# Kernel optimization log

Measured on AMD Instinct MI355X. Metric: run time of the kernel, lower is better.

Reference implementation:

```python
import jax, jax.numpy as jnp
import numpy as np

B, LQ, LT, D = 16, 576, 512, 768
H, DH = 12, 64
TOPK = 64
GATE_INIT = -4.0
EPS = 1e-5


def _layernorm(x, g, b):
    m = jnp.mean(x, axis=-1, keepdims=True)
    v = jnp.mean(jnp.square(x - m), axis=-1, keepdims=True)
    return (x - m) * jax.lax.rsqrt(v + EPS) * g + b


def setup_inputs() -> dict:
    key = jax.random.key(0)
    ks = jax.random.split(key, 8)
    s = D ** -0.5
    return {
        "x_q": jax.random.normal(ks[0], (B, LQ, D), jnp.float32),
        "x_kv": jax.random.normal(ks[1], (B, LT, D), jnp.float32),
        "kv_attn_mask": jnp.ones((B, LT), jnp.int32),
        "wq": jax.random.normal(ks[2], (D, D), jnp.float32) * s,
        "wk": jax.random.normal(ks[3], (D, D), jnp.float32) * s,
        "wv": jax.random.normal(ks[4], (D, D), jnp.float32) * s,
        "wo": jax.random.normal(ks[5], (D, D), jnp.float32) * s,
        "ln_q_g": jnp.ones((D,), jnp.float32),
        "ln_q_b": jnp.zeros((D,), jnp.float32),
        "ln_kv_g": jnp.ones((D,), jnp.float32),
        "ln_kv_b": jnp.zeros((D,), jnp.float32),
        "head_queries": jax.random.normal(ks[6], (H, DH), jnp.float32) * DH ** -0.5,
        "resid_logit": jnp.asarray(GATE_INIT, jnp.float32),
    }


def reference(x_q, x_kv, kv_attn_mask, wq, wk, wv, wo,
              ln_q_g, ln_q_b, ln_kv_g, ln_kv_b, head_queries, resid_logit):
    scale = DH ** -0.5
    Bc, Lq, _ = x_q.shape
    Lt = x_kv.shape[1]
    xq_n = _layernorm(x_q, ln_q_g, ln_q_b)
    xkv_n = _layernorm(x_kv, ln_kv_g, ln_kv_b)
    # torch Linear: y = x @ W.T
    q = (xq_n @ wq.T).reshape(Bc, Lq, H, DH).transpose(0, 2, 1, 3)   # [B,H,Lq,DH]
    k = (xkv_n @ wk.T).reshape(Bc, Lt, H, DH).transpose(0, 2, 1, 3)  # [B,H,Lt,DH]
    v = (xkv_n @ wv.T).reshape(Bc, Lt, H, DH).transpose(0, 2, 1, 3)

    valid = (kv_attn_mask != 0)  # [B,Lt]
    neg = jnp.asarray(-jnp.inf, q.dtype)

    # head-wise gate from learned head queries attending over keys
    gate_scores = jnp.einsum('hd,bhld->bhl', head_queries, k) * scale  # [B,H,Lt]
    gate_scores = jnp.where(valid[:, None, :], gate_scores, neg)
    gate_attn = jax.nn.softmax(gate_scores, axis=-1)
    c_h = jnp.einsum('bhl,bhld->bhd', gate_attn, k)
    g_logits = jnp.einsum('bhd,hd->bh', c_h, head_queries) * scale
    g_h = jax.nn.sigmoid(g_logits)[:, :, None, None]  # [B,H,1,1]

    # top-k token routing: zero out non-selected K/V (matches torch.where -> zeros)
    if TOPK and TOPK < Lt:
        _, topk_idx = jax.lax.top_k(gate_scores, TOPK)  # [B,H,K]
        keep = jax.nn.one_hot(topk_idx, Lt, dtype=q.dtype).sum(axis=-2) > 0  # [B,H,Lt]
        k = jnp.where(keep[..., None], k, 0.0)
        v = jnp.where(keep[..., None], v, 0.0)

    attn_logits = jnp.einsum('bhqd,bhkd->bhqk', q, k) * scale  # [B,H,Lq,Lt]
    attn_logits = jnp.where(valid[:, None, None, :], attn_logits, neg)
    attn = jax.nn.softmax(attn_logits, axis=-1)
    out = jnp.einsum('bhqk,bhkd->bhqd', attn, v) * g_h
    out = out.transpose(0, 2, 1, 3).reshape(Bc, Lq, H * DH)
    out = out @ wo.T
    alpha = jax.nn.sigmoid(resid_logit)
    return x_q + alpha * out
```

## Files before the change

kernel.cpp:

```cpp
#include <hip/hip_runtime.h>
#include <math.h>

#define BB 16
#define LQ 576
#define LT 512
#define DD 768
#define HH 12
#define DH 64
#define TOPK 64

typedef __attribute__((ext_vector_type(8))) short bf16x8;
typedef __attribute__((ext_vector_type(4))) float f32x4;
typedef __attribute__((ext_vector_type(4))) unsigned short u16x4;

static constexpr size_t XQBF  = 0;
static constexpr size_t XKVBF = 3538944;
static constexpr size_t WQB   = 6684672;
static constexpr size_t WKB   = 6979584;
static constexpr size_t WVB   = 7274496;
static constexpr size_t WOB   = 7569408;
static constexpr size_t QBFo  = 7864320;
static constexpr size_t UBo   = 11403264;
static constexpr size_t GSo   = 11409408;
static constexpr size_t IDXo  = 17694720;
static constexpr size_t VBIA  = 17707008;
static constexpr size_t NDVo  = 17719296;
static constexpr size_t GHo   = 17719488;
static constexpr size_t KCo   = 17719680;
static constexpr size_t VCTo  = 18112896;

__device__ inline unsigned short f2bf(float f) {
  union { float f; unsigned u; } v; v.f = f;
  unsigned r = v.u + 0x7FFFu + ((v.u >> 16) & 1u);
  return (unsigned short)(r >> 16);
}
__device__ inline float bf2f(unsigned short u) {
  union { unsigned u; float f; } v; v.u = ((unsigned)u) << 16;
  return v.f;
}
__device__ inline void gload_lds16(const void* src, void* dst) {
  __builtin_amdgcn_global_load_lds((const __attribute__((address_space(1))) void*)src,
                                   (__attribute__((address_space(3))) void*)dst, 16, 0, 0);
}

__global__ __launch_bounds__(256) void ln_all(const float* __restrict__ xq,
                                              const float* __restrict__ xkv,
                                              const float* __restrict__ gq,
                                              const float* __restrict__ bq,
                                              const float* __restrict__ gkv,
                                              const float* __restrict__ bkv,
                                              unsigned short* __restrict__ yq,
                                              unsigned short* __restrict__ ykv) {
  int row = blockIdx.x;
  const float *xr, *gg, *bb;
  unsigned short* yr;
  if (row < BB * LQ) {
    xr = xq + (size_t)row * DD; gg = gq; bb = bq; yr = yq + (size_t)row * DD;
  } else {
    int r = row - BB * LQ;
    xr = xkv + (size_t)r * DD; gg = gkv; bb = bkv; yr = ykv + (size_t)r * DD;
  }
  int t = threadIdx.x;
  float v0 = xr[t], v1 = xr[t + 256], v2 = xr[t + 512];
  __shared__ float red[4];
  float s = v0 + v1 + v2;
  #pragma unroll
  for (int o = 32; o > 0; o >>= 1) s += __shfl_xor(s, o);
  if ((t & 63) == 0) red[t >> 6] = s;
  __syncthreads();
  float m = (red[0] + red[1] + red[2] + red[3]) * (1.0f / 768.0f);
  float d0 = v0 - m, d1 = v1 - m, d2 = v2 - m;
  float s2 = d0 * d0 + d1 * d1 + d2 * d2;
  #pragma unroll
  for (int o = 32; o > 0; o >>= 1) s2 += __shfl_xor(s2, o);
  __syncthreads();
  if ((t & 63) == 0) red[t >> 6] = s2;
  __syncthreads();
  float var = (red[0] + red[1] + red[2] + red[3]) * (1.0f / 768.0f);
  float rs = rsqrtf(var + 1e-5f);
  yr[t]       = f2bf(d0 * rs * gg[t]       + bb[t]);
  yr[t + 256] = f2bf(d1 * rs * gg[t + 256] + bb[t + 256]);
  yr[t + 512] = f2bf(d2 * rs * gg[t + 512] + bb[t + 512]);
}

__global__ __launch_bounds__(256) void conv4u(const float* __restrict__ s0, const float* __restrict__ s1,
                                              const float* __restrict__ s2, const float* __restrict__ s3,
                                              unsigned short* d0, unsigned short* d1,
                                              unsigned short* d2, unsigned short* d3,
                                              const float* __restrict__ hq,
                                              unsigned short* __restrict__ UB) {
  int t = threadIdx.x;
  if (blockIdx.y == 4) {
    int h = blockIdx.x;
    if (h >= 16) return;
    if (h < HH) {
      float a0 = 0.0f, a1 = 0.0f, a2 = 0.0f;
      for (int d = 0; d < DH; ++d) {
        float sc = hq[h * DH + d];
        const float* wr = s1 + (size_t)(h * DH + d) * DD;
        a0 += sc * wr[t]; a1 += sc * wr[t + 256]; a2 += sc * wr[t + 512];
      }
      UB[h * DD + t]       = f2bf(a0 * 0.125f);
      UB[h * DD + t + 256] = f2bf(a1 * 0.125f);
      UB[h * DD + t + 512] = f2bf(a2 * 0.125f);
    } else {
      UB[h * DD + t] = 0; UB[h * DD + t + 256] = 0; UB[h * DD + t + 512] = 0;
    }
    return;
  }
  const float* s; unsigned short* d;
  switch (blockIdx.y) {
    case 0: s = s0; d = d0; break;
    case 1: s = s1; d = d1; break;
    case 2: s = s2; d = d2; break;
    default: s = s3; d = d3; break;
  }
  int i = (blockIdx.x * 256 + t) * 4;
  float4 v = *reinterpret_cast<const float4*>(&s[i]);
  u16x4 o = { f2bf(v.x), f2bf(v.y), f2bf(v.z), f2bf(v.w) };
  *reinterpret_cast<u16x4*>(&d[i]) = o;
}


#define COMMON_PREAMBLE()                                                      \
  const int tid = threadIdx.x;                                                 \
  const int w = tid >> 6, l = tid & 63;                                        \
  const int lq = l & 15, g = l >> 4;                                           \
  const int srow = l >> 3;                                                     \
  const int scol = ((l & 7) * 16) ^ ((srow & 7) << 4);

#define STAGE2(BUFI, T)                                                        \
  {                                                                            \
    int k0s = (T) * 64;                                                        \
    _Pragma("unroll")                                                          \
    for (int it = 0; it < 4; ++it) {                                           \
      int rbase = it * 32 + w * 8;                                             \
      gload_lds16(Asrc + (size_t)rbase * DD + k0s, &As[BUFI][rbase * 64]);     \
      gload_lds16(Bsrc + (size_t)rbase * DD + k0s, &Bs[BUFI][rbase * 64]);     \
    }                                                                          \
  }

#define COMPUTE2(BUFI)                                                         \
  {                                                                            \
    bf16x8 a[4][2], b[4][2];                                                   \
    _Pragma("unroll")                                                          \
    for (int mi = 0; mi < 4; ++mi)                                             \
      _Pragma("unroll")                                                        \
      for (int ks = 0; ks < 2; ++ks) {                                         \
        a[mi][ks] = *reinterpret_cast<const bf16x8*>(&As[BUFI][aoff[mi][ks]]); \
        b[mi][ks] = *reinterpret_cast<const bf16x8*>(&Bs[BUFI][boff[mi][ks]]); \
      }                                                                        \
    _Pragma("unroll")                                                          \
    for (int ks = 0; ks < 2; ++ks)                                             \
      _Pragma("unroll")                                                        \
      for (int mi = 0; mi < 4; ++mi)                                           \
        _Pragma("unroll")                                                      \
        for (int ni = 0; ni < 4; ++ni)                                         \
          acc[mi][ni] = __builtin_amdgcn_mfma_f32_16x16x32_bf16(               \
              a[mi][ks], b[ni][ks], acc[mi][ni], 0, 0, 0);                     \
  }

#define GEMM_MAIN()                                                            \
  int aoff[4][2], boff[4][2];                                                  \
  _Pragma("unroll")                                                            \
  for (int mi = 0; mi < 4; ++mi) {                                             \
    int rowa = wr * 64 + mi * 16 + lq;                                         \
    int rowb = wc * 64 + mi * 16 + lq;                                         \
    _Pragma("unroll")                                                          \
    for (int ks = 0; ks < 2; ++ks) {                                           \
      aoff[mi][ks] = rowa * 64 + (((ks * 64 + g * 16) ^ ((rowa & 7) << 4)) >> 1); \
      boff[mi][ks] = rowb * 64 + (((ks * 64 + g * 16) ^ ((rowb & 7) << 4)) >> 1); \
    }                                                                          \
  }                                                                            \
  STAGE2(0, 0);                                                                \
  STAGE2(1, 1);                                                                \
  _Pragma("unroll")                                                            \
  for (int t = 0; t < 12; ++t) {                                               \
    if (t < 11) asm volatile("s_waitcnt vmcnt(8)" ::: "memory");               \
    else        asm volatile("s_waitcnt vmcnt(0)" ::: "memory");               \
    __builtin_amdgcn_sched_barrier(0);                                         \
    __builtin_amdgcn_s_barrier();                                              \
    if ((t & 1) == 0) { COMPUTE2(0); } else { COMPUTE2(1); }                   \
    __builtin_amdgcn_s_barrier();                                              \
    __builtin_amdgcn_sched_barrier(0);                                         \
    if (t + 2 < 12) {                                                          \
      if ((t & 1) == 0) { STAGE2(0, t + 2); } else { STAGE2(1, t + 2); }       \
    }                                                                          \
  }

__global__ __launch_bounds__(256) void gs_gemm(const unsigned short* __restrict__ xkvb,
                                               const unsigned short* __restrict__ UB,
                                               float* __restrict__ GS) {
  __shared__ __align__(16) unsigned short Xs[2][64 * 64];
  __shared__ __align__(16) unsigned short Us[2][16 * 64];
  COMMON_PREAMBLE();
  const int bm = blockIdx.x * 64;
  const unsigned short* Asrc = xkvb + (size_t)(bm + srow) * DD + (scol >> 1);
  const unsigned short* Us0 = UB + (size_t)srow * DD + (scol >> 1);
  const unsigned short* Us1 = UB + (size_t)(8 + srow) * DD + (scol >> 1);

#define GS_STAGE(BUFI, T)                                                      \
  {                                                                            \
    int k0s = (T) * 64;                                                        \
    _Pragma("unroll")                                                          \
    for (int it = 0; it < 2; ++it) {                                           \
      int rbase = it * 32 + w * 8;                                             \
      gload_lds16(Asrc + (size_t)rbase * DD + k0s, &Xs[BUFI][rbase * 64]);     \
    }                                                                          \
    gload_lds16(Us0 + k0s, &Us[BUFI][0]);                                      \
    gload_lds16(Us1 + k0s, &Us[BUFI][8 * 64]);                                 \
  }

  f32x4 acc = {};

#define GS_COMPUTE(BUFI)                                                       \
  {                                                                            \
    _Pragma("unroll")                                                          \
    for (int ks = 0; ks < 2; ++ks) {                                           \
      int arow = w * 16 + lq;                                                  \
      int acb = (ks * 64 + g * 16) ^ ((arow & 7) << 4);                        \
      bf16x8 a = *reinterpret_cast<const bf16x8*>(&Xs[BUFI][arow * 64 + (acb >> 1)]); \
      int brow = lq;                                                           \
      int bcb = (ks * 64 + g * 16) ^ ((brow & 7) << 4);                        \
      bf16x8 b = *reinterpret_cast<const bf16x8*>(&Us[BUFI][brow * 64 + (bcb >> 1)]); \
      acc = __builtin_amdgcn_mfma_f32_16x16x32_bf16(a, b, acc, 0, 0, 0);       \
    }                                                                          \
  }

  GS_STAGE(0, 0);
  GS_STAGE(1, 1);
  #pragma unroll
  for (int t = 0; t < 12; ++t) {
    if (t < 11) asm volatile("s_waitcnt vmcnt(4)" ::: "memory");
    else        asm volatile("s_waitcnt vmcnt(0)" ::: "memory");
    __builtin_amdgcn_sched_barrier(0);
    __builtin_amdgcn_s_barrier();
    if ((t & 1) == 0) { GS_COMPUTE(0); } else { GS_COMPUTE(1); }
    __builtin_amdgcn_s_barrier();
    __builtin_amdgcn_sched_barrier(0);
    if (t + 2 < 12) {
      if ((t & 1) == 0) { GS_STAGE(0, t + 2); } else { GS_STAGE(1, t + 2); }
    }
  }
  #pragma unroll
  for (int r = 0; r < 4; ++r)
    GS[(size_t)(bm + w * 16 + g * 4 + r) * 16 + lq] = acc[r];
}

__global__ __launch_bounds__(512) void gate_topk(const float* __restrict__ GS,
                                                 const int* __restrict__ mask,
                                                 int* __restrict__ idxo,
                                                 float* __restrict__ vbias,
                                                 float* __restrict__ ndv,
                                                 float* __restrict__ g_h) {
  int bh = blockIdx.x, b = bh / HH, h = bh % HH;
  int l = threadIdx.x;
  __shared__ float s_sc[512];
  __shared__ float red[8];
  __shared__ int wred[8];
  float sc = GS[(size_t)(b * LT + l) * 16 + h];
  bool maskv = (mask[b * LT + l] != 0);
  if (!maskv) sc = -INFINITY;
  s_sc[l] = sc;
  float m0 = sc;
  #pragma unroll
  for (int o = 32; o > 0; o >>= 1) m0 = fmaxf(m0, __shfl_xor(m0, o));
  if ((l & 63) == 0) red[l >> 6] = m0;
  __syncthreads();
  float m = red[0];
  #pragma unroll
  for (int w = 1; w < 8; w++) m = fmaxf(m, red[w]);
  float p = __expf(sc - m);
  float s1 = p;
  #pragma unroll
  for (int o = 32; o > 0; o >>= 1) s1 += __shfl_xor(s1, o);
  __syncthreads();
  if ((l & 63) == 0) red[l >> 6] = s1;
  __syncthreads();
  float Z = 0.0f;
  #pragma unroll
  for (int w = 0; w < 8; w++) Z += red[w];
  p /= Z;
  float gc = maskv ? p * sc : 0.0f;
  #pragma unroll
  for (int o = 32; o > 0; o >>= 1) gc += __shfl_xor(gc, o);
  __syncthreads();
  if ((l & 63) == 0) red[l >> 6] = gc;
  __syncthreads();
  if (l == 0) {
    float G = 0.0f;
    #pragma unroll
    for (int w = 0; w < 8; w++) G += red[w];
    g_h[bh] = 1.0f / (1.0f + __expf(-G));
  }
  float my = s_sc[l];
  int cnt = 0;
  for (int j = 0; j < LT; j++) {
    float sj = s_sc[j];
    cnt += (sj > my || (sj == my && j < l)) ? 1 : 0;
  }
  if (cnt < TOPK) {
    idxo[bh * TOPK + cnt] = l;
    vbias[bh * TOPK + cnt] = maskv ? 0.0f : -INFINITY;
  }
  int dv = (maskv && cnt >= TOPK) ? 1 : 0;
  unsigned long long bal = __ballot(dv);
  if ((l & 63) == 0) wred[l >> 6] = __popcll(bal);
  __syncthreads();
  if (l == 0) {
    int nd = 0;
    #pragma unroll
    for (int w = 0; w < 8; w++) nd += wred[w];
    ndv[bh] = (float)nd;
  }
}

__global__ __launch_bounds__(256, 2) void proj2(const unsigned short* __restrict__ xqb,
                                                const unsigned short* __restrict__ wqb,
                                                const unsigned short* __restrict__ xkvb,
                                                const unsigned short* __restrict__ wkb,
                                                const unsigned short* __restrict__ wvb,
                                                const int* __restrict__ idxo,
                                                unsigned short* __restrict__ QBF,
                                                unsigned short* __restrict__ KC,
                                                unsigned short* __restrict__ VCT) {
  __shared__ __align__(16) unsigned short As[2][128 * 64];
  __shared__ __align__(16) unsigned short Bs[2][128 * 64];
  __shared__ int sidx[64];
  COMMON_PREAMBLE();
  int p = blockIdx.x;
  int bid = (p & 7) * 78 + (p >> 3);

  if (bid < 432) {
    const int wr = w >> 1, wc = w & 1;
    const int mtile = bid / 6, nt = bid % 6;
    const int bm = mtile * 128, bn = nt * 128;
    const unsigned short* Asrc = xqb + (size_t)(bm + srow) * DD + (scol >> 1);
    const unsigned short* Bsrc = wqb + (size_t)(bn + srow) * DD + (scol >> 1);
    f32x4 acc[4][4] = {};
    GEMM_MAIN();
    const int m_base = bm + wr * 64, n_base = bn + wc * 64;
    #pragma unroll
    for (int mi = 0; mi < 4; ++mi)
      #pragma unroll
      for (int r = 0; r < 4; ++r) {
        int m = m_base + mi * 16 + g * 4 + r;
        #pragma unroll
        for (int ni = 0; ni < 4; ++ni) {
          int n = n_base + ni * 16 + lq;
          QBF[(size_t)m * DD + n] = f2bf(acc[mi][ni][r] * 0.125f);
        }
      }
  } else {
    const int bh = bid - 432, b = bh / HH, h = bh % HH;
    if (tid < 64) sidx[tid] = idxo[bh * TOPK + tid];
    __syncthreads();
    unsigned short* Xs0 = &As[0][0]; unsigned short* Xs1 = &As[0][4096];
    unsigned short* Kp0 = &As[1][0]; unsigned short* Kp1 = &As[1][4096];
    unsigned short* Vp0 = &Bs[0][0]; unsigned short* Vp1 = &Bs[0][4096];
    const int j0 = w * 16 + srow, j1 = w * 16 + 8 + srow;
    const unsigned short* xs0 = xkvb + (size_t)(b * LT + sidx[j0]) * DD + (scol >> 1);
    const unsigned short* xs1 = xkvb + (size_t)(b * LT + sidx[j1]) * DD + (scol >> 1);
    const unsigned short* wk0 = wkb + (size_t)(h * DH + j0) * DD + (scol >> 1);
    const unsigned short* wk1 = wkb + (size_t)(h * DH + j1) * DD + (scol >> 1);
    const unsigned short* wv0 = wvb + (size_t)(h * DH + j0) * DD + (scol >> 1);
    const unsigned short* wv1 = wvb + (size_t)(h * DH + j1) * DD + (scol >> 1);

#define KV_STAGE(Xd, Kd, Vd, T)                                                \
    {                                                                          \
      int k0s = (T) * 64;                                                      \
      gload_lds16(xs0 + k0s, Xd + (w * 16) * 64);                              \
      gload_lds16(xs1 + k0s, Xd + (w * 16 + 8) * 64);                          \
      gload_lds16(wk0 + k0s, Kd + (w * 16) * 64);                              \
      gload_lds16(wk1 + k0s, Kd + (w * 16 + 8) * 64);                          \
      gload_lds16(wv0 + k0s, Vd + (w * 16) * 64);                              \
      gload_lds16(wv1 + k0s, Vd + (w * 16 + 8) * 64);                          \
    }

    f32x4 accK[4] = {}, accV[4] = {};

#define KV_COMPUTE(Xd, Kd, Vd)                                                 \
    {                                                                          \
      _Pragma("unroll")                                                        \
      for (int ks = 0; ks < 2; ++ks) {                                         \
        int arow = w * 16 + lq;                                                \
        int acb = (ks * 64 + g * 16) ^ ((arow & 7) << 4);                      \
        bf16x8 ax = *reinterpret_cast<const bf16x8*>(&Xd[arow * 64 + (acb >> 1)]); \
        bf16x8 av = *reinterpret_cast<const bf16x8*>(&Vd[arow * 64 + (acb >> 1)]); \
        _Pragma("unroll")                                                      \
        for (int ni = 0; ni < 4; ++ni) {                                       \
          int brow = ni * 16 + lq;                                             \
          int bcb = (ks * 64 + g * 16) ^ ((brow & 7) << 4);                    \
          bf16x8 bk = *reinterpret_cast<const bf16x8*>(&Kd[brow * 64 + (bcb >> 1)]); \
          accK[ni] = __builtin_amdgcn_mfma_f32_16x16x32_bf16(ax, bk, accK[ni], 0, 0, 0); \
          bf16x8 bx = *reinterpret_cast<const bf16x8*>(&Xd[brow * 64 + (bcb >> 1)]); \
          accV[ni] = __builtin_amdgcn_mfma_f32_16x16x32_bf16(av, bx, accV[ni], 0, 0, 0); \
        }                                                                      \
      }                                                                        \
    }

    KV_STAGE(Xs0, Kp0, Vp0, 0);
    KV_STAGE(Xs1, Kp1, Vp1, 1);
    #pragma unroll
    for (int t = 0; t < 12; ++t) {
      if (t < 11) asm volatile("s_waitcnt vmcnt(6)" ::: "memory");
      else        asm volatile("s_waitcnt vmcnt(0)" ::: "memory");
      __builtin_amdgcn_sched_barrier(0);
      __builtin_amdgcn_s_barrier();
      if ((t & 1) == 0) { KV_COMPUTE(Xs0, Kp0, Vp0); } else { KV_COMPUTE(Xs1, Kp1, Vp1); }
      __builtin_amdgcn_s_barrier();
      __builtin_amdgcn_sched_barrier(0);
      if (t + 2 < 12) {
        if ((t & 1) == 0) { KV_STAGE(Xs0, Kp0, Vp0, t + 2); } else { KV_STAGE(Xs1, Kp1, Vp1, t + 2); }
      }
    }
    #pragma unroll
    for (int ni = 0; ni < 4; ++ni)
      #pragma unroll
      for (int r = 0; r < 4; ++r) {
        int mrow = w * 16 + g * 4 + r;
        KC [(size_t)bh * 4096 + mrow * 64 + ni * 16 + lq] = f2bf(accK[ni][r]);
        VCT[(size_t)bh * 4096 + mrow * 64 + ni * 16 + lq] = f2bf(accV[ni][r]);
      }
  }
}

__global__ __launch_bounds__(256, 2) void o_gemm(const unsigned short* __restrict__ ABF,
                                                 const unsigned short* __restrict__ wob,
                                                 float* __restrict__ out,
                                                 const float* __restrict__ resid,
                                                 const float* __restrict__ gl) {
  __shared__ __align__(16) unsigned short As[2][128 * 64];
  __shared__ __align__(16) unsigned short Bs[2][128 * 64];
  COMMON_PREAMBLE();
  const int wr = w >> 1, wc = w & 1;
  int p = blockIdx.x;
  int bid = (p & 7) * 54 + (p >> 3);
  const int mtile = bid / 6, nt = bid % 6;
  const int bm = mtile * 128, bn = nt * 128;
  const unsigned short* Asrc = ABF + (size_t)(bm + srow) * DD + (scol >> 1);
  const unsigned short* Bsrc = wob + (size_t)(bn + srow) * DD + (scol >> 1);

  f32x4 acc[4][4] = {};
  GEMM_MAIN();

  float alpha = 1.0f / (1.0f + __expf(-gl[0]));
  const int m_base = bm + wr * 64, n_base = bn + wc * 64;
  #pragma unroll
  for (int mi = 0; mi < 4; ++mi)
    #pragma unroll
    for (int r = 0; r < 4; ++r) {
      int m = m_base + mi * 16 + g * 4 + r;
      #pragma unroll
      for (int ni = 0; ni < 4; ++ni) {
        int n = n_base + ni * 16 + lq;
        out[(size_t)m * DD + n] = resid[(size_t)m * DD + n] + alpha * acc[mi][ni][r];
      }
    }
}

__global__ __launch_bounds__(256) void attn_topk(const unsigned short* __restrict__ Qb,
                                                 const unsigned short* __restrict__ KC,
                                                 const unsigned short* __restrict__ VCT,
                                                 const float* __restrict__ vbias,
                                                 const float* __restrict__ ndv,
                                                 const float* __restrict__ g_h,
                                                 unsigned short* __restrict__ att) {
  const int bh = blockIdx.y, b = bh / HH, h = bh % HH;
  const int q0 = blockIdx.x * 64;
  const int tid = threadIdx.x;
  const int w = tid >> 6, l = tid & 63;
  const int lq = l & 15, g = l >> 4;

  __shared__ __align__(16) unsigned short Klds[64 * 64];
  __shared__ __align__(16) unsigned short Vlds[64 * 64];
  __shared__ float svb[64];

  const int srow = l >> 3;
  const int scol = ((l & 7) * 16) ^ ((srow & 7) << 4);
  #pragma unroll
  for (int it = 0; it < 2; ++it) {
    int rbase = w * 16 + it * 8;
    gload_lds16(KC  + (size_t)bh * 4096 + (rbase + srow) * 64 + (scol >> 1), &Klds[rbase * 64]);
    gload_lds16(VCT + (size_t)bh * 4096 + (rbase + srow) * 64 + (scol >> 1), &Vlds[rbase * 64]);
  }
  if (tid < 64) svb[tid] = vbias[bh * TOPK + tid];

  bf16x8 qf0, qf1;
  {
    const unsigned short* qrow =
        Qb + ((size_t)(b * LQ + q0 + w * 16 + lq)) * DD + h * DH + g * 8;
    qf0 = *reinterpret_cast<const bf16x8*>(qrow);
    qf1 = *reinterpret_cast<const bf16x8*>(qrow + 32);
  }
  __syncthreads();

  f32x4 S[4];
  #pragma unroll
  for (int kt = 0; kt < 4; ++kt) {
    f32x4 acc = {};
    int row = kt * 16 + lq;
    int c0 = (g * 16) ^ ((row & 7) << 4);
    int c1 = (64 + g * 16) ^ ((row & 7) << 4);
    bf16x8 a0 = *reinterpret_cast<const bf16x8*>(&Klds[row * 64 + (c0 >> 1)]);
    bf16x8 a1 = *reinterpret_cast<const bf16x8*>(&Klds[row * 64 + (c1 >> 1)]);
    acc = __builtin_amdgcn_mfma_f32_16x16x32_bf16(a0, qf0, acc, 0, 0, 0);
    acc = __builtin_amdgcn_mfma_f32_16x16x32_bf16(a1, qf1, acc, 0, 0, 0);
    S[kt] = acc;
  }

  float s_v[16];
  float mx = -INFINITY;
  #pragma unroll
  for (int kt = 0; kt < 4; ++kt)
    #pragma unroll
    for (int r = 0; r < 4; ++r) {
      float s = S[kt][r] + svb[kt * 16 + g * 4 + r];
      s_v[kt * 4 + r] = s;
      mx = fmaxf(mx, s);
    }
  mx = fmaxf(mx, __shfl_xor(mx, 16));
  mx = fmaxf(mx, __shfl_xor(mx, 32));
  float nd = ndv[bh];
  float m2 = (nd > 0.0f) ? fmaxf(mx, 0.0f) : mx;

  float psum = 0.0f;
  unsigned short pb[16];
  #pragma unroll
  for (int i = 0; i < 16; ++i) {
    float p = __expf(s_v[i] - m2);
    psum += p;
    pb[i] = f2bf(p);
  }
  psum += __shfl_xor(psum, 16);
  psum += __shfl_xor(psum, 32);
  float Z = psum + nd * __expf(-m2);
  float inv = 1.0f / Z;

  bf16x8 pa0, pa1;
  #pragma unroll
  for (int j = 0; j < 8; ++j) { pa0[j] = (short)pb[j]; pa1[j] = (short)pb[8 + j]; }

  f32x4 O[4] = {};
  #pragma unroll
  for (int dt = 0; dt < 4; ++dt) {
    int r = dt * 16 + lq;
    int swz = (r & 7) << 4;
    #pragma unroll
    for (int ks = 0; ks < 2; ++ks) {
      int cl = (64 * ks + g * 8) ^ swz;
      int ch = (64 * ks + 32 + g * 8) ^ swz;
      u16x4 lo = *reinterpret_cast<const u16x4*>(&Vlds[r * 64 + (cl >> 1)]);
      u16x4 hi = *reinterpret_cast<const u16x4*>(&Vlds[r * 64 + (ch >> 1)]);
      bf16x8 vb = { (short)lo[0], (short)lo[1], (short)lo[2], (short)lo[3],
                    (short)hi[0], (short)hi[1], (short)hi[2], (short)hi[3] };
      O[dt] = __builtin_amdgcn_mfma_f32_16x16x32_bf16(ks == 0 ? pa0 : pa1, vb, O[dt], 0, 0, 0);
    }
  }

  float invl[4];
  #pragma unroll
  for (int r = 0; r < 4; ++r) invl[r] = __shfl(inv, g * 4 + r);
  float gh = g_h[bh];
  #pragma unroll
  for (int dt = 0; dt < 4; ++dt)
    #pragma unroll
    for (int r = 0; r < 4; ++r) {
      int q = q0 + w * 16 + g * 4 + r;
      att[((size_t)(b * LQ + q)) * DD + h * DH + dt * 16 + lq] =
          f2bf(O[dt][r] * invl[r] * gh);
    }
}

extern "C" void kernel_launch(void* const* d_in, const int* in_sizes, int n_in,
                              void* d_out, int out_size, void* d_ws, size_t ws_size,
                              hipStream_t stream) {
  const float* x_q      = (const float*)d_in[0];
  const float* x_kv     = (const float*)d_in[1];
  const int*   mask     = (const int*)d_in[2];
  const float* wq       = (const float*)d_in[3];
  const float* wk       = (const float*)d_in[4];
  const float* wv       = (const float*)d_in[5];
  const float* wo       = (const float*)d_in[6];
  const float* ln_q_g   = (const float*)d_in[7];
  const float* ln_q_b   = (const float*)d_in[8];
  const float* ln_kv_g  = (const float*)d_in[9];
  const float* ln_kv_b  = (const float*)d_in[10];
  const float* hq       = (const float*)d_in[11];
  const float* resid_l  = (const float*)d_in[12];
  float* out = (float*)d_out;
  float* ws  = (float*)d_ws;

  unsigned short* xqb  = (unsigned short*)(ws + XQBF);
  unsigned short* xkvb = (unsigned short*)(ws + XKVBF);
  unsigned short* wqb  = (unsigned short*)(ws + WQB);
  unsigned short* wkb  = (unsigned short*)(ws + WKB);
  unsigned short* wvb  = (unsigned short*)(ws + WVB);
  unsigned short* wob  = (unsigned short*)(ws + WOB);
  unsigned short* QBF  = (unsigned short*)(ws + QBFo);
  unsigned short* UB   = (unsigned short*)(ws + UBo);
  float*          GS   = (float*)(ws + GSo);
  int*            IDX  = (int*)(ws + IDXo);
  unsigned short* KC   = (unsigned short*)(ws + KCo);
  unsigned short* VCT  = (unsigned short*)(ws + VCTo);
  unsigned short* ABF  = xqb;

  conv4u<<<dim3(576, 5), dim3(256), 0, stream>>>(wq, wk, wv, wo, wqb, wkb, wvb, wob, hq, UB);

  ln_all<<<dim3(BB * LQ + BB * LT), dim3(256), 0, stream>>>(x_q, x_kv, ln_q_g, ln_q_b,
                                                            ln_kv_g, ln_kv_b, xqb, xkvb);

  gs_gemm<<<dim3(128), dim3(256), 0, stream>>>(xkvb, UB, GS);

  gate_topk<<<dim3(BB * HH), dim3(512), 0, stream>>>(GS, mask, IDX,
                                                     ws + VBIA, ws + NDVo, ws + GHo);

  proj2<<<dim3(624), dim3(256), 0, stream>>>(xqb, wqb, xkvb, wkb, wvb, IDX, QBF, KC, VCT);

  attn_topk<<<dim3(LQ / 64, BB * HH), dim3(256), 0, stream>>>(QBF, KC, VCT,
                                                              ws + VBIA, ws + NDVo, ws + GHo, ABF);

  o_gemm<<<dim3(432), dim3(256), 0, stream>>>(ABF, wob, out, x_q, resid_l);
}
```

Baseline: 110.5 us.

## Split fused Q/KV projection kernel and shrink Q/O GEMM tiles to 64x128

The fused proj2 kernel, which ran the Q projection and the gathered top-k K/V projection in one launch, is split into a dedicated q_gemm and a separate kvc_gemm. Q and O GEMMs now use 64x128 tiles with each wave computing 32x64, which doubles the block count to 864 and raises the occupancy hint to 3 blocks per CU. The aim is better load balance and more waves in flight on the many-CU device. In exchange it adds an extra kernel launch and lowers per-block data reuse because the tiles are smaller.

```diff
diff --git a/kernel.cpp b/kernel.cpp
--- a/kernel.cpp
+++ b/kernel.cpp
@@ -121,7 +121,6 @@
   *reinterpret_cast<u16x4*>(&d[i]) = o;
 }
 
-
 #define COMMON_PREAMBLE()                                                      \
   const int tid = threadIdx.x;                                                 \
   const int w = tid >> 6, l = tid & 63;                                        \
@@ -129,64 +128,132 @@
   const int srow = l >> 3;                                                     \
   const int scol = ((l & 7) * 16) ^ ((srow & 7) << 4);
 
-#define STAGE2(BUFI, T)                                                        \
+
+#define QO_STAGE(BUFI, T)                                                      \
   {                                                                            \
     int k0s = (T) * 64;                                                        \
     _Pragma("unroll")                                                          \
-    for (int it = 0; it < 4; ++it) {                                           \
-      int rbase = it * 32 + w * 8;                                             \
-      gload_lds16(Asrc + (size_t)rbase * DD + k0s, &As[BUFI][rbase * 64]);     \
-      gload_lds16(Bsrc + (size_t)rbase * DD + k0s, &Bs[BUFI][rbase * 64]);     \
-    }                                                                          \
-  }
-
-#define COMPUTE2(BUFI)                                                         \
+    for (int it = 0; it < 2; ++it)                                             \
+      gload_lds16(Asrc + (size_t)it * 8 * DD + k0s, &As[BUFI][(w * 16 + it * 8) * 64]); \
+    _Pragma("unroll")                                                          \
+    for (int jt = 0; jt < 4; ++jt)                                             \
+      gload_lds16(Bsrc + (size_t)jt * 8 * DD + k0s, &Bs[BUFI][(w * 32 + jt * 8) * 64]); \
+  }
+
+#define QO_COMPUTE(BUFI)                                                       \
   {                                                                            \
-    bf16x8 a[4][2], b[4][2];                                                   \
-    _Pragma("unroll")                                                          \
-    for (int mi = 0; mi < 4; ++mi)                                             \
+    bf16x8 a[2][2], b[4][2];                                                   \
+    _Pragma("unroll")                                                          \
+    for (int mi = 0; mi < 2; ++mi)                                             \
       _Pragma("unroll")                                                        \
-      for (int ks = 0; ks < 2; ++ks) {                                         \
+      for (int ks = 0; ks < 2; ++ks)                                           \
         a[mi][ks] = *reinterpret_cast<const bf16x8*>(&As[BUFI][aoff[mi][ks]]); \
-        b[mi][ks] = *reinterpret_cast<const bf16x8*>(&Bs[BUFI][boff[mi][ks]]); \
-      }                                                                        \
+    _Pragma("unroll")                                                          \
+    for (int ni = 0; ni < 4; ++ni)                                             \
+      _Pragma("unroll")                                                        \
+      for (int ks = 0; ks < 2; ++ks)                                           \
+        b[ni][ks] = *reinterpret_cast<const bf16x8*>(&Bs[BUFI][boff[ni][ks]]); \
     _Pragma("unroll")                                                          \
     for (int ks = 0; ks < 2; ++ks)                                             \
       _Pragma("unroll")                                                        \
-      for (int mi = 0; mi < 4; ++mi)                                           \
+      for (int mi = 0; mi < 2; ++mi)                                           \
         _Pragma("unroll")                                                      \
         for (int ni = 0; ni < 4; ++ni)                                         \
           acc[mi][ni] = __builtin_amdgcn_mfma_f32_16x16x32_bf16(               \
               a[mi][ks], b[ni][ks], acc[mi][ni], 0, 0, 0);                     \
   }
 
-#define GEMM_MAIN()                                                            \
-  int aoff[4][2], boff[4][2];                                                  \
+#define QO_MAIN()                                                              \
+  const int wr = w >> 1, wc = w & 1;                                           \
+  int aoff[2][2], boff[4][2];                                                  \
   _Pragma("unroll")                                                            \
-  for (int mi = 0; mi < 4; ++mi) {                                             \
-    int rowa = wr * 64 + mi * 16 + lq;                                         \
-    int rowb = wc * 64 + mi * 16 + lq;                                         \
-    _Pragma("unroll")                                                          \
-    for (int ks = 0; ks < 2; ++ks) {                                           \
+  for (int mi = 0; mi < 2; ++mi) {                                             \
+    int rowa = wr * 32 + mi * 16 + lq;                                         \
+    _Pragma("unroll")                                                          \
+    for (int ks = 0; ks < 2; ++ks)                                             \
       aoff[mi][ks] = rowa * 64 + (((ks * 64 + g * 16) ^ ((rowa & 7) << 4)) >> 1); \
-      boff[mi][ks] = rowb * 64 + (((ks * 64 + g * 16) ^ ((rowb & 7) << 4)) >> 1); \
-    }                                                                          \
   }                                                                            \
-  STAGE2(0, 0);                                                                \
-  STAGE2(1, 1);                                                                \
+  _Pragma("unroll")                                                            \
+  for (int ni = 0; ni < 4; ++ni) {                                             \
+    int rowb = wc * 64 + ni * 16 + lq;                                         \
+    _Pragma("unroll")                                                          \
+    for (int ks = 0; ks < 2; ++ks)                                             \
+      boff[ni][ks] = rowb * 64 + (((ks * 64 + g * 16) ^ ((rowb & 7) << 4)) >> 1); \
+  }                                                                            \
+  QO_STAGE(0, 0);                                                              \
+  QO_STAGE(1, 1);                                                              \
   _Pragma("unroll")                                                            \
   for (int t = 0; t < 12; ++t) {                                               \
-    if (t < 11) asm volatile("s_waitcnt vmcnt(8)" ::: "memory");               \
+    if (t < 11) asm volatile("s_waitcnt vmcnt(6)" ::: "memory");               \
     else        asm volatile("s_waitcnt vmcnt(0)" ::: "memory");               \
     __builtin_amdgcn_sched_barrier(0);                                         \
     __builtin_amdgcn_s_barrier();                                              \
-    if ((t & 1) == 0) { COMPUTE2(0); } else { COMPUTE2(1); }                   \
+    if ((t & 1) == 0) { QO_COMPUTE(0); } else { QO_COMPUTE(1); }               \
     __builtin_amdgcn_s_barrier();                                              \
     __builtin_amdgcn_sched_barrier(0);                                         \
     if (t + 2 < 12) {                                                          \
-      if ((t & 1) == 0) { STAGE2(0, t + 2); } else { STAGE2(1, t + 2); }       \
+      if ((t & 1) == 0) { QO_STAGE(0, t + 2); } else { QO_STAGE(1, t + 2); }   \
     }                                                                          \
   }
+
+__global__ __launch_bounds__(256, 3) void q_gemm(const unsigned short* __restrict__ xqb,
+                                                 const unsigned short* __restrict__ wqb,
+                                                 unsigned short* __restrict__ QBF) {
+  __shared__ __align__(16) unsigned short As[2][64 * 64];
+  __shared__ __align__(16) unsigned short Bs[2][128 * 64];
+  COMMON_PREAMBLE();
+  int p = blockIdx.x;
+  int bid = (p & 7) * 108 + (p >> 3);
+  const int mtile = bid / 6, nt = bid % 6;
+  const int bm = mtile * 64, bn = nt * 128;
+  const unsigned short* Asrc = xqb + (size_t)(bm + w * 16 + srow) * DD + (scol >> 1);
+  const unsigned short* Bsrc = wqb + (size_t)(bn + w * 32 + srow) * DD + (scol >> 1);
+  f32x4 acc[2][4] = {};
+  QO_MAIN();
+  const int m_base = bm + wr * 32, n_base = bn + wc * 64;
+  #pragma unroll
+  for (int mi = 0; mi < 2; ++mi)
+    #pragma unroll
+    for (int r = 0; r < 4; ++r) {
+      int m = m_base + mi * 16 + g * 4 + r;
+      #pragma unroll
+      for (int ni = 0; ni < 4; ++ni) {
+        int n = n_base + ni * 16 + lq;
+        QBF[(size_t)m * DD + n] = f2bf(acc[mi][ni][r] * 0.125f);
+      }
+    }
+}
+
+__global__ __launch_bounds__(256, 3) void o_gemm(const unsigned short* __restrict__ ABF,
+                                                 const unsigned short* __restrict__ wob,
+                                                 float* __restrict__ out,
+                                                 const float* __restrict__ resid,
+                                                 const float* __restrict__ gl) {
+  __shared__ __align__(16) unsigned short As[2][64 * 64];
+  __shared__ __align__(16) unsigned short Bs[2][128 * 64];
+  COMMON_PREAMBLE();
+  int p = blockIdx.x;
+  int bid = (p & 7) * 108 + (p >> 3);
+  const int mtile = bid / 6, nt = bid % 6;
+  const int bm = mtile * 64, bn = nt * 128;
+  const unsigned short* Asrc = ABF + (size_t)(bm + w * 16 + srow) * DD + (scol >> 1);
+  const unsigned short* Bsrc = wob + (size_t)(bn + w * 32 + srow) * DD + (scol >> 1);
+  f32x4 acc[2][4] = {};
+  QO_MAIN();
+  float alpha = 1.0f / (1.0f + __expf(-gl[0]));
+  const int m_base = bm + wr * 32, n_base = bn + wc * 64;
+  #pragma unroll
+  for (int mi = 0; mi < 2; ++mi)
+    #pragma unroll
+    for (int r = 0; r < 4; ++r) {
+      int m = m_base + mi * 16 + g * 4 + r;
+      #pragma unroll
+      for (int ni = 0; ni < 4; ++ni) {
+        int n = n_base + ni * 16 + lq;
+        out[(size_t)m * DD + n] = resid[(size_t)m * DD + n] + alpha * acc[mi][ni][r];
+      }
+    }
+}
 
 __global__ __launch_bounds__(256) void gs_gemm(const unsigned short* __restrict__ xkvb,
                                                const unsigned short* __restrict__ UB,
@@ -315,147 +382,83 @@
   }
 }
 
-__global__ __launch_bounds__(256, 2) void proj2(const unsigned short* __restrict__ xqb,
-                                                const unsigned short* __restrict__ wqb,
-                                                const unsigned short* __restrict__ xkvb,
-                                                const unsigned short* __restrict__ wkb,
-                                                const unsigned short* __restrict__ wvb,
-                                                const int* __restrict__ idxo,
-                                                unsigned short* __restrict__ QBF,
-                                                unsigned short* __restrict__ KC,
-                                                unsigned short* __restrict__ VCT) {
-  __shared__ __align__(16) unsigned short As[2][128 * 64];
-  __shared__ __align__(16) unsigned short Bs[2][128 * 64];
+__global__ __launch_bounds__(256, 2) void kvc_gemm(const unsigned short* __restrict__ xkvb,
+                                                   const unsigned short* __restrict__ wkb,
+                                                   const unsigned short* __restrict__ wvb,
+                                                   const int* __restrict__ idxo,
+                                                   unsigned short* __restrict__ KC,
+                                                   unsigned short* __restrict__ VCT) {
+  __shared__ __align__(16) unsigned short Xs[2][4096];
+  __shared__ __align__(16) unsigned short Ks[2][4096];
+  __shared__ __align__(16) unsigned short Vs[2][4096];
   __shared__ int sidx[64];
   COMMON_PREAMBLE();
-  int p = blockIdx.x;
-  int bid = (p & 7) * 78 + (p >> 3);
-
-  if (bid < 432) {
-    const int wr = w >> 1, wc = w & 1;
-    const int mtile = bid / 6, nt = bid % 6;
-    const int bm = mtile * 128, bn = nt * 128;
-    const unsigned short* Asrc = xqb + (size_t)(bm + srow) * DD + (scol >> 1);
-    const unsigned short* Bsrc = wqb + (size_t)(bn + srow) * DD + (scol >> 1);
-    f32x4 acc[4][4] = {};
-    GEMM_MAIN();
-    const int m_base = bm + wr * 64, n_base = bn + wc * 64;
-    #pragma unroll
-    for (int mi = 0; mi < 4; ++mi)
-      #pragma unroll
-      for (int r = 0; r < 4; ++r) {
-        int m = m_base + mi * 16 + g * 4 + r;
-        #pragma unroll
-        for (int ni = 0; ni < 4; ++ni) {
-          int n = n_base + ni * 16 + lq;
-          QBF[(size_t)m * DD + n] = f2bf(acc[mi][ni][r] * 0.125f);
-        }
-      }
-  } else {
-    const int bh = bid - 432, b = bh / HH, h = bh % HH;
-    if (tid < 64) sidx[tid] = idxo[bh * TOPK + tid];
-    __syncthreads();
-    unsigned short* Xs0 = &As[0][0]; unsigned short* Xs1 = &As[0][4096];
-    unsigned short* Kp0 = &As[1][0]; unsigned short* Kp1 = &As[1][4096];
-    unsigned short* Vp0 = &Bs[0][0]; unsigned short* Vp1 = &Bs[0][4096];
-    const int j0 = w * 16 + srow, j1 = w * 16 + 8 + srow;
-    const unsigned short* xs0 = xkvb + (size_t)(b * LT + sidx[j0]) * DD + (scol >> 1);
-    const unsigned short* xs1 = xkvb + (size_t)(b * LT + sidx[j1]) * DD + (scol >> 1);
-    const unsigned short* wk0 = wkb + (size_t)(h * DH + j0) * DD + (scol >> 1);
-    const unsigned short* wk1 = wkb + (size_t)(h * DH + j1) * DD + (scol >> 1);
-    const unsigned short* wv0 = wvb + (size_t)(h * DH + j0) * DD + (scol >> 1);
-    const unsigned short* wv1 = wvb + (size_t)(h * DH + j1) * DD + (scol >> 1);
-
-#define KV_STAGE(Xd, Kd, Vd, T)                                                \
+  const int bh = blockIdx.x, b = bh / HH, h = bh % HH;
+  if (tid < 64) sidx[tid] = idxo[bh * TOPK + tid];
+  __syncthreads();
+  const int j0 = w * 16 + srow, j1 = w * 16 + 8 + srow;
+  const unsigned short* xs0 = xkvb + (size_t)(b * LT + sidx[j0]) * DD + (scol >> 1);
+  const unsigned short* xs1 = xkvb + (size_t)(b * LT + sidx[j1]) * DD + (scol >> 1);
+  const unsigned short* wk0 = wkb + (size_t)(h * DH + j0) * DD + (scol >> 1);
+  const unsigned short* wk1 = wkb + (size_t)(h * DH + j1) * DD + (scol >> 1);
+  const unsigned short* wv0 = wvb + (size_t)(h * DH + j0) * DD + (scol >> 1);
+  const unsigned short* wv1 = wvb + (size_t)(h * DH + j1) * DD + (scol >> 1);
+
+#define KV_STAGE(BUFI, T)                                                      \
     {                                                                          \
       int k0s = (T) * 64;                                                      \
-      gload_lds16(xs0 + k0s, Xd + (w * 16) * 64);                              \
-      gload_lds16(xs1 + k0s, Xd + (w * 16 + 8) * 64);                          \
-      gload_lds16(wk0 + k0s, Kd + (w * 16) * 64);                              \
-      gload_lds16(wk1 + k0s, Kd + (w * 16 + 8) * 64);                          \
-      gload_lds16(wv0 + k0s, Vd + (w * 16) * 64);                              \
-      gload_lds16(wv1 + k0s, Vd + (w * 16 + 8) * 64);                          \
-    }
-
-    f32x4 accK[4] = {}, accV[4] = {};
-
-#define KV_COMPUTE(Xd, Kd, Vd)                                                 \
+      gload_lds16(xs0 + k0s, &Xs[BUFI][(w * 16) * 64]);                        \
+      gload_lds16(xs1 + k0s, &Xs[BUFI][(w * 16 + 8) * 64]);                    \
+      gload_lds16(wk0 + k0s, &Ks[BUFI][(w * 16) * 64]);                        \
+      gload_lds16(wk1 + k0s, &Ks[BUFI][(w * 16 + 8) * 64]);                    \
+      gload_lds16(wv0 + k0s, &Vs[BUFI][(w * 16) * 64]);                        \
+      gload_lds16(wv1 + k0s, &Vs[BUFI][(w * 16 + 8) * 64]);                    \
+    }
+
+  f32x4 accK[4] = {}, accV[4] = {};
+
+#define KV_COMPUTE(BUFI)                                                       \
     {                                                                          \
       _Pragma("unroll")                                                        \
       for (int ks = 0; ks < 2; ++ks) {                                         \
         int arow = w * 16 + lq;                                                \
         int acb = (ks * 64 + g * 16) ^ ((arow & 7) << 4);                      \
-        bf16x8 ax = *reinterpret_cast<const bf16x8*>(&Xd[arow * 64 + (acb >> 1)]); \
-        bf16x8 av = *reinterpret_cast<const bf16x8*>(&Vd[arow * 64 + (acb >> 1)]); \
+        bf16x8 ax = *reinterpret_cast<const bf16x8*>(&Xs[BUFI][arow * 64 + (acb >> 1)]); \
+        bf16x8 av = *reinterpret_cast<const bf16x8*>(&Vs[BUFI][arow * 64 + (acb >> 1)]); \
         _Pragma("unroll")                                                      \
         for (int ni = 0; ni < 4; ++ni) {                                       \
           int brow = ni * 16 + lq;                                             \
           int bcb = (ks * 64 + g * 16) ^ ((brow & 7) << 4);                    \
-          bf16x8 bk = *reinterpret_cast<const bf16x8*>(&Kd[brow * 64 + (bcb >> 1)]); \
+          bf16x8 bk = *reinterpret_cast<const bf16x8*>(&Ks[BUFI][brow * 64 + (bcb >> 1)]); \
           accK[ni] = __builtin_amdgcn_mfma_f32_16x16x32_bf16(ax, bk, accK[ni], 0, 0, 0); \
-          bf16x8 bx = *reinterpret_cast<const bf16x8*>(&Xd[brow * 64 + (bcb >> 1)]); \
+          bf16x8 bx = *reinterpret_cast<const bf16x8*>(&Xs[BUFI][brow * 64 + (bcb >> 1)]); \
           accV[ni] = __builtin_amdgcn_mfma_f32_16x16x32_bf16(av, bx, accV[ni], 0, 0, 0); \
         }                                                                      \
       }                                                                        \
     }
 
-    KV_STAGE(Xs0, Kp0, Vp0, 0);
-    KV_STAGE(Xs1, Kp1, Vp1, 1);
-    #pragma unroll
-    for (int t = 0; t < 12; ++t) {
-      if (t < 11) asm volatile("s_waitcnt vmcnt(6)" ::: "memory");
-      else        asm volatile("s_waitcnt vmcnt(0)" ::: "memory");
-      __builtin_amdgcn_sched_barrier(0);
-      __builtin_amdgcn_s_barrier();
-      if ((t & 1) == 0) { KV_COMPUTE(Xs0, Kp0, Vp0); } else { KV_COMPUTE(Xs1, Kp1, Vp1); }
-      __builtin_amdgcn_s_barrier();
-      __builtin_amdgcn_sched_barrier(0);
-      if (t + 2 < 12) {
-        if ((t & 1) == 0) { KV_STAGE(Xs0, Kp0, Vp0, t + 2); } else { KV_STAGE(Xs1, Kp1, Vp1, t + 2); }
-      }
-    }
-    #pragma unroll
-    for (int ni = 0; ni < 4; ++ni)
-      #pragma unroll
-      for (int r = 0; r < 4; ++r) {
-        int mrow = w * 16 + g * 4 + r;
-        KC [(size_t)bh * 4096 + mrow * 64 + ni * 16 + lq] = f2bf(accK[ni][r]);
-        VCT[(size_t)bh * 4096 + mrow * 64 + ni * 16 + lq] = f2bf(accV[ni][r]);
-      }
-  }
-}
-
-__global__ __launch_bounds__(256, 2) void o_gemm(const unsigned short* __restrict__ ABF,
-                                                 const unsigned short* __restrict__ wob,
-                                                 float* __restrict__ out,
-                                                 const float* __restrict__ resid,
-                                                 const float* __restrict__ gl) {
-  __shared__ __align__(16) unsigned short As[2][128 * 64];
-  __shared__ __align__(16) unsigned short Bs[2][128 * 64];
-  COMMON_PREAMBLE();
-  const int wr = w >> 1, wc = w & 1;
-  int p = blockIdx.x;
-  int bid = (p & 7) * 54 + (p >> 3);
-  const int mtile = bid / 6, nt = bid % 6;
-  const int bm = mtile * 128, bn = nt * 128;
-  const unsigned short* Asrc = ABF + (size_t)(bm + srow) * DD + (scol >> 1);
-  const unsigned short* Bsrc = wob + (size_t)(bn + srow) * DD + (scol >> 1);
-
-  f32x4 acc[4][4] = {};
-  GEMM_MAIN();
-
-  float alpha = 1.0f / (1.0f + __expf(-gl[0]));
-  const int m_base = bm + wr * 64, n_base = bn + wc * 64;
-  #pragma unroll
-  for (int mi = 0; mi < 4; ++mi)
+  KV_STAGE(0, 0);
+  KV_STAGE(1, 1);
+  #pragma unroll
+  for (int t = 0; t < 12; ++t) {
+    if (t < 11) asm volatile("s_waitcnt vmcnt(6)" ::: "memory");
+    else        asm volatile("s_waitcnt vmcnt(0)" ::: "memory");
+    __builtin_amdgcn_sched_barrier(0);
+    __builtin_amdgcn_s_barrier();
+    if ((t & 1) == 0) { KV_COMPUTE(0); } else { KV_COMPUTE(1); }
+    __builtin_amdgcn_s_barrier();
+    __builtin_amdgcn_sched_barrier(0);
+    if (t + 2 < 12) {
+      if ((t & 1) == 0) { KV_STAGE(0, t + 2); } else { KV_STAGE(1, t + 2); }
+    }
+  }
+  #pragma unroll
+  for (int ni = 0; ni < 4; ++ni)
     #pragma unroll
     for (int r = 0; r < 4; ++r) {
-      int m = m_base + mi * 16 + g * 4 + r;
-      #pragma unroll
-      for (int ni = 0; ni < 4; ++ni) {
-        int n = n_base + ni * 16 + lq;
-        out[(size_t)m * DD + n] = resid[(size_t)m * DD + n] + alpha * acc[mi][ni][r];
-      }
+      int mrow = w * 16 + g * 4 + r;
+      KC [(size_t)bh * 4096 + mrow * 64 + ni * 16 + lq] = f2bf(accK[ni][r]);
+      VCT[(size_t)bh * 4096 + mrow * 64 + ni * 16 + lq] = f2bf(accV[ni][r]);
     }
 }
 
@@ -615,10 +618,12 @@
   gate_topk<<<dim3(BB * HH), dim3(512), 0, stream>>>(GS, mask, IDX,
                                                      ws + VBIA, ws + NDVo, ws + GHo);
 
-  proj2<<<dim3(624), dim3(256), 0, stream>>>(xqb, wqb, xkvb, wkb, wvb, IDX, QBF, KC, VCT);
+  q_gemm<<<dim3(864), dim3(256), 0, stream>>>(xqb, wqb, QBF);
+
+  kvc_gemm<<<dim3(BB * HH), dim3(256), 0, stream>>>(xkvb, wkb, wvb, IDX, KC, VCT);
 
   attn_topk<<<dim3(LQ / 64, BB * HH), dim3(256), 0, stream>>>(QBF, KC, VCT,
                                                               ws + VBIA, ws + NDVo, ws + GHo, ABF);
 
-  o_gemm<<<dim3(432), dim3(256), 0, stream>>>(ABF, wob, out, x_q, resid_l);
-}
+  o_gemm<<<dim3(864), dim3(256), 0, stream>>>(ABF, wob, out, x_q, resid_l);
+}
```

Measured after the change: 119.8 us. 1.08x slower.
